# Performance work log

Measured on AMD Instinct MI355X. Metric: run time of the kernel, lower is better.

Reference implementation:

```python
import jax, jax.numpy as jnp
import numpy as np

B, N, F = 64, 512, 128

def setup_inputs() -> dict:
    key = jax.random.key(0)
    k1, k2 = jax.random.split(key)
    inp = jax.random.normal(k1, (B, N, F), dtype=jnp.float32)
    valid_mask = jnp.ones((B, N, N), dtype=jnp.float32)
    weight = 0.1 * jax.random.normal(k2, (N, N), dtype=jnp.float32)
    return {"input": inp, "valid_mask": valid_mask, "weight": weight}

def reference(input, valid_mask, weight):
    # softmax over last dim of weight, broadcast over batch
    adj = jax.nn.softmax(weight, axis=-1)[None, :, :] * valid_mask  # [B,N,N]
    n = weight.shape[0]
    adj = adj + jnp.eye(n, dtype=adj.dtype)[None, :, :]
    # symmetric degree normalization D^-1/2 A D^-1/2 (D diagonal of row sums).
    # Original builds dense D and does two matmuls; diagonal scaling is the
    # identical math expressed as row/col broadcast.
    row_sum = adj.sum(axis=2)  # [B,N]
    d = jnp.where(row_sum > 0, jax.lax.rsqrt(row_sum), 0.0)  # inf -> 0 handling
    adj_nor = d[:, :, None] * adj * d[:, None, :]  # [B,N,N]
    return jnp.matmul(adj_nor, input)  # [B,N,F]
```

## Files before the change

### kernel.cpp

```cpp
#include <hip/hip_runtime.h>
#include <math.h>

#define BB 64
#define NN 512
#define FF 128
#define ASTR 72
#define PADT 129
#define TI2 16

typedef __bf16 bf16x8 __attribute__((ext_vector_type(8)));
typedef float floatx4 __attribute__((ext_vector_type(4)));

__device__ __forceinline__ unsigned int bf16u(float f) {
    unsigned int u = __builtin_bit_cast(unsigned int, f);
    unsigned int r = (u + 0x7FFFu + ((u >> 16) & 1u)) >> 16;
    return r & 0xFFFFu;
}

__global__ __launch_bounds__(256) void softmax_rowsum_kernel(
        const float* __restrict__ w, const float* __restrict__ mask,
        float* __restrict__ S, float* __restrict__ dvec) {
    __shared__ float Srow[NN];
    __shared__ float red[8];
    const int row = blockIdx.x;
    const int bg = blockIdx.y;
    const int tid = threadIdx.x;
    const int wv = tid >> 6, lane = tid & 63;

    float v0 = w[(size_t)row * NN + tid];
    float v1 = w[(size_t)row * NN + tid + 256];

    float m = fmaxf(v0, v1);
    #pragma unroll
    for (int off = 32; off > 0; off >>= 1)
        m = fmaxf(m, __shfl_down(m, off, 64));
    if (lane == 0) red[wv] = m;
    __syncthreads();
    if (tid == 0) red[4] = fmaxf(fmaxf(red[0], red[1]), fmaxf(red[2], red[3]));
    __syncthreads();
    m = red[4];

    float e0 = expf(v0 - m);
    float e1 = expf(v1 - m);
    float s = e0 + e1;
    #pragma unroll
    for (int off = 32; off > 0; off >>= 1)
        s += __shfl_down(s, off, 64);
    __syncthreads();
    if (lane == 0) red[wv] = s;
    __syncthreads();
    if (tid == 0) red[5] = 1.0f / (red[0] + red[1] + red[2] + red[3]);
    __syncthreads();
    const float inv = red[5];
    const float s0v = e0 * inv, s1v = e1 * inv;

    Srow[tid] = s0v;
    Srow[tid + 256] = s1v;
    if (bg == 0) {
        S[(size_t)row * NN + tid] = s0v;
        S[(size_t)row * NN + tid + 256] = s1v;
    }
    __syncthreads();

    float4 sA = *(const float4*)&Srow[lane * 8];
    float4 sB = *(const float4*)&Srow[lane * 8 + 4];

    float4 mA[4], mB[4];
    #pragma unroll
    for (int t = 0; t < 4; ++t) {
        int b = bg * 16 + wv * 4 + t;
        const float4* mrow = (const float4*)(mask + ((size_t)b * NN + row) * NN);
        mA[t] = mrow[2 * lane];
        mB[t] = mrow[2 * lane + 1];
    }
    #pragma unroll
    for (int t = 0; t < 4; ++t) {
        float sum = mA[t].x * sA.x + mA[t].y * sA.y + mA[t].z * sA.z + mA[t].w * sA.w
                  + mB[t].x * sB.x + mB[t].y * sB.y + mB[t].z * sB.z + mB[t].w * sB.w;
        #pragma unroll
        for (int off = 32; off > 0; off >>= 1)
            sum += __shfl_down(sum, off, 64);
        if (lane == 0) {
            int b = bg * 16 + wv * 4 + t;
            float rs = sum + 1.0f;
            dvec[b * NN + row] = (rs > 0.f) ? (1.0f / sqrtf(rs)) : 0.f;
        }
    }
}

__global__ __launch_bounds__(256) void xt_kernel(const float* __restrict__ in,
                                                 const float* __restrict__ dvec,
                                                 unsigned short* __restrict__ Xt) {
    __shared__ unsigned short T[64 * PADT];
    const int b = blockIdx.y;
    const int j0 = blockIdx.x * 64;
    const int tid = threadIdx.x;

    const int fg = tid & 31;
    const int jr = tid >> 5;
    #pragma unroll
    for (int p = 0; p < 8; ++p) {
        int j = jr + 8 * p;
        float dj = dvec[b * NN + j0 + j];
        float4 xv = *(const float4*)(in + ((size_t)b * NN + j0 + j) * FF + 4 * fg);
        T[j * PADT + 4 * fg + 0] = (unsigned short)bf16u(xv.x * dj);
        T[j * PADT + 4 * fg + 1] = (unsigned short)bf16u(xv.y * dj);
        T[j * PADT + 4 * fg + 2] = (unsigned short)bf16u(xv.z * dj);
        T[j * PADT + 4 * fg + 3] = (unsigned short)bf16u(xv.w * dj);
    }
    __syncthreads();
    const int c = tid & 7;
    const int fr = tid >> 3;
    #pragma unroll
    for (int q = 0; q < 4; ++q) {
        int f = fr + 32 * q;
        unsigned int v01 = (unsigned int)T[(8 * c + 0) * PADT + f] |
                           ((unsigned int)T[(8 * c + 1) * PADT + f] << 16);
        unsigned int v23 = (unsigned int)T[(8 * c + 2) * PADT + f] |
                           ((unsigned int)T[(8 * c + 3) * PADT + f] << 16);
        unsigned int v45 = (unsigned int)T[(8 * c + 4) * PADT + f] |
                           ((unsigned int)T[(8 * c + 5) * PADT + f] << 16);
        unsigned int v67 = (unsigned int)T[(8 * c + 6) * PADT + f] |
                           ((unsigned int)T[(8 * c + 7) * PADT + f] << 16);
        *(uint4*)(Xt + ((size_t)b * FF + f) * NN + j0 + 8 * c) = make_uint4(v01, v23, v45, v67);
    }
}

__global__ __launch_bounds__(256) void matmul_kernel(
        const float* __restrict__ S, const float* __restrict__ mask,
        const float* __restrict__ dvec, const unsigned short* __restrict__ Xt,
        const float* __restrict__ in, float* __restrict__ out) {
    __shared__ __align__(16) unsigned short Alds[2][TI2 * ASTR];

    const int b = blockIdx.y;
    const int i_base = blockIdx.x * TI2;
    const int tid = threadIdx.x;
    const int wv = tid >> 6;
    const int lane = tid & 63;
    const int quad = lane >> 4;
    const int l16 = lane & 15;
    const int fw = wv * 32;

    const float* dB = dvec + b * NN;
    const unsigned short* XtB = Xt + (size_t)b * FF * NN;

    floatx4 acc[2];
    acc[0] = (floatx4){0.f, 0.f, 0.f, 0.f};
    acc[1] = (floatx4){0.f, 0.f, 0.f, 0.f};

    const int a_il = tid >> 4;
    const int a_js = (tid & 15) * 4;
    const float* mbase = mask + ((size_t)b * NN + i_base + a_il) * NN + a_js;
    const float* sbase = S + (size_t)(i_base + a_il) * NN + a_js;

    {
        float4 m0 = *(const float4*)mbase;
        float4 s0 = *(const float4*)sbase;
        uint2 pk;
        pk.x = bf16u(m0.x * s0.x) | (bf16u(m0.y * s0.y) << 16);
        pk.y = bf16u(m0.z * s0.z) | (bf16u(m0.w * s0.w) << 16);
        *(uint2*)(&Alds[0][0] + a_il * ASTR + a_js) = pk;
    }
    bf16x8 bcur[4];
    #pragma unroll
    for (int s = 0; s < 2; ++s)
        #pragma unroll
        for (int nt = 0; nt < 2; ++nt)
            bcur[s * 2 + nt] = *(const bf16x8*)&XtB[(size_t)(fw + nt * 16 + l16) * NN + s * 32 + quad * 8];

    #pragma unroll
    for (int c = 0; c < 8; ++c) {
        const int p = c & 1;
        float4 m0, s0;
        if (c < 7) {
            m0 = *(const float4*)(mbase + (c + 1) * 64);
            s0 = *(const float4*)(sbase + (c + 1) * 64);
        }
        __syncthreads();

        bf16x8 bnxt[4];
        if (c < 7) {
            int jn = (c + 1) * 64;
            #pragma unroll
            for (int s = 0; s < 2; ++s)
                #pragma unroll
                for (int nt = 0; nt < 2; ++nt)
                    bnxt[s * 2 + nt] = *(const bf16x8*)&XtB[(size_t)(fw + nt * 16 + l16) * NN + jn + s * 32 + quad * 8];
        }

        #pragma unroll
        for (int s = 0; s < 2; ++s) {
            bf16x8 af = *(const bf16x8*)&Alds[p][l16 * ASTR + s * 32 + quad * 8];
            #pragma unroll
            for (int nt = 0; nt < 2; ++nt)
                acc[nt] = __builtin_amdgcn_mfma_f32_16x16x32_bf16(af, bcur[s * 2 + nt], acc[nt], 0, 0, 0);
        }

        if (c < 7) {
            uint2 pk;
            pk.x = bf16u(m0.x * s0.x) | (bf16u(m0.y * s0.y) << 16);
            pk.y = bf16u(m0.z * s0.z) | (bf16u(m0.w * s0.w) << 16);
            *(uint2*)(&Alds[p ^ 1][0] + a_il * ASTR + a_js) = pk;
            #pragma unroll
            for (int q = 0; q < 4; ++q) bcur[q] = bnxt[q];
        }
    }

    #pragma unroll
    for (int nt = 0; nt < 2; ++nt) {
        int f = fw + nt * 16 + l16;
        #pragma unroll
        for (int r = 0; r < 4; ++r) {
            int i = i_base + quad * 4 + r;
            float di = dB[i];
            float x = in[((size_t)b * NN + i) * FF + f];
            out[((size_t)b * NN + i) * FF + f] = di * (acc[nt][r] + di * x);
        }
    }
}

extern "C" void kernel_launch(void* const* d_in, const int* in_sizes, int n_in,
                              void* d_out, int out_size, void* d_ws, size_t ws_size,
                              hipStream_t stream) {
    const float* inp  = (const float*)d_in[0];
    const float* mask = (const float*)d_in[1];
    const float* w    = (const float*)d_in[2];
    float* out = (float*)d_out;

    unsigned short* Xt = (unsigned short*)d_ws;
    float* S    = (float*)(Xt + (size_t)BB * FF * NN);
    float* dvec = S + (size_t)NN * NN;

    softmax_rowsum_kernel<<<dim3(NN, 4), 256, 0, stream>>>(w, mask, S, dvec);
    xt_kernel<<<dim3(NN / 64, BB), 256, 0, stream>>>(inp, dvec, Xt);
    matmul_kernel<<<dim3(NN / TI2, BB), 256, 0, stream>>>(S, mask, dvec, Xt, inp, out);
}
```

Before: 147.3 us.

## Load A fragments directly from global memory, drop LDS staging and barriers

The matmul kernel no longer stages the masked softmax tile through double-buffered shared memory. Each wave now loads mask and S straight from global memory into its MFMA A-fragment layout, converting to bf16 with a native cast, and the __syncthreads barriers are gone. The aim is to remove LDS traffic and synchronisation. The cost is that all four waves in a block load the same A tile redundantly (4x mask/S reads, mostly from cache), and the explicit software prefetch is replaced by compiler unrolling.

Result: slower. 197.6 us (+34.2%).

```diff
diff --git a/kernel.cpp b/kernel.cpp
--- a/kernel.cpp
+++ b/kernel.cpp
@@ -4,9 +4,7 @@
 #define BB 64
 #define NN 512
 #define FF 128
-#define ASTR 72
 #define PADT 129
-#define TI2 16
 
 typedef __bf16 bf16x8 __attribute__((ext_vector_type(8)));
 typedef float floatx4 __attribute__((ext_vector_type(4)));
@@ -130,91 +128,58 @@
         const float* __restrict__ S, const float* __restrict__ mask,
         const float* __restrict__ dvec, const unsigned short* __restrict__ Xt,
         const float* __restrict__ in, float* __restrict__ out) {
-    __shared__ __align__(16) unsigned short Alds[2][TI2 * ASTR];
-
     const int b = blockIdx.y;
-    const int i_base = blockIdx.x * TI2;
+    const int i_base = blockIdx.x * 16;
     const int tid = threadIdx.x;
     const int wv = tid >> 6;
     const int lane = tid & 63;
-    const int quad = lane >> 4;
-    const int l16 = lane & 15;
+    const int q = lane >> 4;
+    const int r = lane & 15;
     const int fw = wv * 32;
 
+    const float* mrow = mask + ((size_t)b * NN + i_base + r) * NN + q * 8;
+    const float* srow = S + (size_t)(i_base + r) * NN + q * 8;
+    const unsigned short* xb0 = Xt + ((size_t)b * FF + fw + r) * NN + q * 8;
+    const unsigned short* xb1 = xb0 + (size_t)16 * NN;
+
+    floatx4 acc0 = (floatx4){0.f, 0.f, 0.f, 0.f};
+    floatx4 acc1 = (floatx4){0.f, 0.f, 0.f, 0.f};
+
+    #pragma unroll 4
+    for (int s = 0; s < 16; ++s) {
+        const int o = s * 32;
+        float4 ma0 = *(const float4*)(mrow + o);
+        float4 ma1 = *(const float4*)(mrow + o + 4);
+        float4 sa0 = *(const float4*)(srow + o);
+        float4 sa1 = *(const float4*)(srow + o + 4);
+        bf16x8 b0 = *(const bf16x8*)(xb0 + o);
+        bf16x8 b1 = *(const bf16x8*)(xb1 + o);
+
+        bf16x8 af;
+        af[0] = (__bf16)(ma0.x * sa0.x);
+        af[1] = (__bf16)(ma0.y * sa0.y);
+        af[2] = (__bf16)(ma0.z * sa0.z);
+        af[3] = (__bf16)(ma0.w * sa0.w);
+        af[4] = (__bf16)(ma1.x * sa1.x);
+        af[5] = (__bf16)(ma1.y * sa1.y);
+        af[6] = (__bf16)(ma1.z * sa1.z);
+        af[7] = (__bf16)(ma1.w * sa1.w);
+
+        acc0 = __builtin_amdgcn_mfma_f32_16x16x32_bf16(af, b0, acc0, 0, 0, 0);
+        acc1 = __builtin_amdgcn_mfma_f32_16x16x32_bf16(af, b1, acc1, 0, 0, 0);
+    }
+
     const float* dB = dvec + b * NN;
-    const unsigned short* XtB = Xt + (size_t)b * FF * NN;
-
-    floatx4 acc[2];
-    acc[0] = (floatx4){0.f, 0.f, 0.f, 0.f};
-    acc[1] = (floatx4){0.f, 0.f, 0.f, 0.f};
-
-    const int a_il = tid >> 4;
-    const int a_js = (tid & 15) * 4;
-    const float* mbase = mask + ((size_t)b * NN + i_base + a_il) * NN + a_js;
-    const float* sbase = S + (size_t)(i_base + a_il) * NN + a_js;
-
-    {
-        float4 m0 = *(const float4*)mbase;
-        float4 s0 = *(const float4*)sbase;
-        uint2 pk;
-        pk.x = bf16u(m0.x * s0.x) | (bf16u(m0.y * s0.y) << 16);
-        pk.y = bf16u(m0.z * s0.z) | (bf16u(m0.w * s0.w) << 16);
-        *(uint2*)(&Alds[0][0] + a_il * ASTR + a_js) = pk;
-    }
-    bf16x8 bcur[4];
-    #pragma unroll
-    for (int s = 0; s < 2; ++s)
+    #pragma unroll
+    for (int nt = 0; nt < 2; ++nt) {
+        int f = fw + nt * 16 + r;
+        const floatx4& a = nt ? acc1 : acc0;
         #pragma unroll
-        for (int nt = 0; nt < 2; ++nt)
-            bcur[s * 2 + nt] = *(const bf16x8*)&XtB[(size_t)(fw + nt * 16 + l16) * NN + s * 32 + quad * 8];
-
-    #pragma unroll
-    for (int c = 0; c < 8; ++c) {
-        const int p = c & 1;
-        float4 m0, s0;
-        if (c < 7) {
-            m0 = *(const float4*)(mbase + (c + 1) * 64);
-            s0 = *(const float4*)(sbase + (c + 1) * 64);
-        }
-        __syncthreads();
-
-        bf16x8 bnxt[4];
-        if (c < 7) {
-            int jn = (c + 1) * 64;
-            #pragma unroll
-            for (int s = 0; s < 2; ++s)
-                #pragma unroll
-                for (int nt = 0; nt < 2; ++nt)
-                    bnxt[s * 2 + nt] = *(const bf16x8*)&XtB[(size_t)(fw + nt * 16 + l16) * NN + jn + s * 32 + quad * 8];
-        }
-
-        #pragma unroll
-        for (int s = 0; s < 2; ++s) {
-            bf16x8 af = *(const bf16x8*)&Alds[p][l16 * ASTR + s * 32 + quad * 8];
-            #pragma unroll
-            for (int nt = 0; nt < 2; ++nt)
-                acc[nt] = __builtin_amdgcn_mfma_f32_16x16x32_bf16(af, bcur[s * 2 + nt], acc[nt], 0, 0, 0);
-        }
-
-        if (c < 7) {
-            uint2 pk;
-            pk.x = bf16u(m0.x * s0.x) | (bf16u(m0.y * s0.y) << 16);
-            pk.y = bf16u(m0.z * s0.z) | (bf16u(m0.w * s0.w) << 16);
-            *(uint2*)(&Alds[p ^ 1][0] + a_il * ASTR + a_js) = pk;
-            #pragma unroll
-            for (int q = 0; q < 4; ++q) bcur[q] = bnxt[q];
-        }
-    }
-
-    #pragma unroll
-    for (int nt = 0; nt < 2; ++nt) {
-        int f = fw + nt * 16 + l16;
-        #pragma unroll
-        for (int r = 0; r < 4; ++r) {
-            int i = i_base + quad * 4 + r;
+        for (int rr = 0; rr < 4; ++rr) {
+            int i = i_base + q * 4 + rr;
             float di = dB[i];
             float x = in[((size_t)b * NN + i) * FF + f];
-            out[((size_t)b * NN + i) * FF + f] = di * (acc[nt][r] + di * x);
+            out[((size_t)b * NN + i) * FF + f] = di * (a[rr] + di * x);
         }
     }
 }
@@ -233,5 +198,5 @@
 
     softmax_rowsum_kernel<<<dim3(NN, 4), 256, 0, stream>>>(w, mask, S, dvec);
     xt_kernel<<<dim3(NN / 64, BB), 256, 0, stream>>>(inp, dvec, Xt);
-    matmul_kernel<<<dim3(NN / TI2, BB), 256, 0, stream>>>(S, mask, dvec, Xt, inp, out);
-}
+    matmul_kernel<<<dim3(NN / 16, BB), 256, 0, stream>>>(S, mask, dvec, Xt, inp, out);
+}
```

## Materialize masked softmax adjacency as bf16 in the row-sum kernel

Applied to the files above, without the earlier changes.

The row-sum kernel now forms the masked softmax products, packs them to bf16 and writes a per-batch adjacency array A to workspace while computing the degree sums. The matmul kernel then loads pre-packed bf16 A tiles directly, instead of re-reading the fp32 mask and the softmax matrix and converting them in its inner loop. This drops the second fp32 pass over the mask in the matmul kernel. In exchange it adds a 32 MB bf16 write and a later read of the same data, so total traffic is roughly unchanged unless A stays resident in the large last-level cache.

Measured after the change: 153.0 us. 1.04x slower.

```diff
diff --git a/kernel.cpp b/kernel.cpp
--- a/kernel.cpp
+++ b/kernel.cpp
@@ -17,9 +17,9 @@
     return r & 0xFFFFu;
 }
 
-__global__ __launch_bounds__(256) void softmax_rowsum_kernel(
+__global__ __launch_bounds__(256) void softmax_rowsum_A_kernel(
         const float* __restrict__ w, const float* __restrict__ mask,
-        float* __restrict__ S, float* __restrict__ dvec) {
+        unsigned short* __restrict__ A, float* __restrict__ dvec) {
     __shared__ float Srow[NN];
     __shared__ float red[8];
     const int row = blockIdx.x;
@@ -52,14 +52,9 @@
     if (tid == 0) red[5] = 1.0f / (red[0] + red[1] + red[2] + red[3]);
     __syncthreads();
     const float inv = red[5];
-    const float s0v = e0 * inv, s1v = e1 * inv;
-
-    Srow[tid] = s0v;
-    Srow[tid + 256] = s1v;
-    if (bg == 0) {
-        S[(size_t)row * NN + tid] = s0v;
-        S[(size_t)row * NN + tid + 256] = s1v;
-    }
+
+    Srow[tid] = e0 * inv;
+    Srow[tid + 256] = e1 * inv;
     __syncthreads();
 
     float4 sA = *(const float4*)&Srow[lane * 8];
@@ -75,13 +70,24 @@
     }
     #pragma unroll
     for (int t = 0; t < 4; ++t) {
-        float sum = mA[t].x * sA.x + mA[t].y * sA.y + mA[t].z * sA.z + mA[t].w * sA.w
-                  + mB[t].x * sB.x + mB[t].y * sB.y + mB[t].z * sB.z + mB[t].w * sB.w;
+        int b = bg * 16 + wv * 4 + t;
+        float p0 = mA[t].x * sA.x, p1 = mA[t].y * sA.y;
+        float p2 = mA[t].z * sA.z, p3 = mA[t].w * sA.w;
+        float p4 = mB[t].x * sB.x, p5 = mB[t].y * sB.y;
+        float p6 = mB[t].z * sB.z, p7 = mB[t].w * sB.w;
+
+        uint4 pk;
+        pk.x = bf16u(p0) | (bf16u(p1) << 16);
+        pk.y = bf16u(p2) | (bf16u(p3) << 16);
+        pk.z = bf16u(p4) | (bf16u(p5) << 16);
+        pk.w = bf16u(p6) | (bf16u(p7) << 16);
+        *(uint4*)(A + ((size_t)b * NN + row) * NN + lane * 8) = pk;
+
+        float sum = p0 + p1 + p2 + p3 + p4 + p5 + p6 + p7;
         #pragma unroll
         for (int off = 32; off > 0; off >>= 1)
             sum += __shfl_down(sum, off, 64);
         if (lane == 0) {
-            int b = bg * 16 + wv * 4 + t;
             float rs = sum + 1.0f;
             dvec[b * NN + row] = (rs > 0.f) ? (1.0f / sqrtf(rs)) : 0.f;
         }
@@ -127,9 +133,9 @@
 }
 
 __global__ __launch_bounds__(256) void matmul_kernel(
-        const float* __restrict__ S, const float* __restrict__ mask,
-        const float* __restrict__ dvec, const unsigned short* __restrict__ Xt,
-        const float* __restrict__ in, float* __restrict__ out) {
+        const unsigned short* __restrict__ A, const float* __restrict__ dvec,
+        const unsigned short* __restrict__ Xt, const float* __restrict__ in,
+        float* __restrict__ out) {
     __shared__ __align__(16) unsigned short Alds[2][TI2 * ASTR];
 
     const int b = blockIdx.y;
@@ -150,17 +156,10 @@
 
     const int a_il = tid >> 4;
     const int a_js = (tid & 15) * 4;
-    const float* mbase = mask + ((size_t)b * NN + i_base + a_il) * NN + a_js;
-    const float* sbase = S + (size_t)(i_base + a_il) * NN + a_js;
-
-    {
-        float4 m0 = *(const float4*)mbase;
-        float4 s0 = *(const float4*)sbase;
-        uint2 pk;
-        pk.x = bf16u(m0.x * s0.x) | (bf16u(m0.y * s0.y) << 16);
-        pk.y = bf16u(m0.z * s0.z) | (bf16u(m0.w * s0.w) << 16);
-        *(uint2*)(&Alds[0][0] + a_il * ASTR + a_js) = pk;
-    }
+    const unsigned short* abase = A + ((size_t)b * NN + i_base + a_il) * NN + a_js;
+
+    *(uint2*)(&Alds[0][0] + a_il * ASTR + a_js) = *(const uint2*)abase;
+
     bf16x8 bcur[4];
     #pragma unroll
     for (int s = 0; s < 2; ++s)
@@ -171,11 +170,8 @@
     #pragma unroll
     for (int c = 0; c < 8; ++c) {
         const int p = c & 1;
-        float4 m0, s0;
-        if (c < 7) {
-            m0 = *(const float4*)(mbase + (c + 1) * 64);
-            s0 = *(const float4*)(sbase + (c + 1) * 64);
-        }
+        uint2 av;
+        if (c < 7) av = *(const uint2*)(abase + (c + 1) * 64);
         __syncthreads();
 
         bf16x8 bnxt[4];
@@ -197,10 +193,7 @@
         }
 
         if (c < 7) {
-            uint2 pk;
-            pk.x = bf16u(m0.x * s0.x) | (bf16u(m0.y * s0.y) << 16);
-            pk.y = bf16u(m0.z * s0.z) | (bf16u(m0.w * s0.w) << 16);
-            *(uint2*)(&Alds[p ^ 1][0] + a_il * ASTR + a_js) = pk;
+            *(uint2*)(&Alds[p ^ 1][0] + a_il * ASTR + a_js) = av;
             #pragma unroll
             for (int q = 0; q < 4; ++q) bcur[q] = bnxt[q];
         }
@@ -227,11 +220,11 @@
     const float* w    = (const float*)d_in[2];
     float* out = (float*)d_out;
 
-    unsigned short* Xt = (unsigned short*)d_ws;
-    float* S    = (float*)(Xt + (size_t)BB * FF * NN);
-    float* dvec = S + (size_t)NN * NN;
-
-    softmax_rowsum_kernel<<<dim3(NN, 4), 256, 0, stream>>>(w, mask, S, dvec);
+    unsigned short* A  = (unsigned short*)d_ws;
+    unsigned short* Xt = A + (size_t)BB * NN * NN;
+    float* dvec = (float*)(Xt + (size_t)BB * FF * NN);
+
+    softmax_rowsum_A_kernel<<<dim3(NN, 4), 256, 0, stream>>>(w, mask, A, dvec);
     xt_kernel<<<dim3(NN / 64, BB), 256, 0, stream>>>(inp, dvec, Xt);
-    matmul_kernel<<<dim3(NN / TI2, BB), 256, 0, stream>>>(S, mask, dvec, Xt, inp, out);
-}
+    matmul_kernel<<<dim3(NN / TI2, BB), 256, 0, stream>>>(A, dvec, Xt, inp, out);
+}
```
